# Kernel tuning notes

Hardware: AMD Instinct MI355X
Metric: run time of the kernel (lower is better)

## Reference

```python
import jax, jax.numpy as jnp
import numpy as np

D_MODEL = 2048
N_HEAD = 16
N_KV_HEAD = 4
D_HEAD = D_MODEL // N_HEAD  # 128
WINDOW = 512
B, T = 2, 2048


def _rope_tables(T, d_head, base=10000.0):
    inv = 1.0 / (base ** (np.arange(0, d_head, 2, dtype=np.float32) / d_head))
    t = np.arange(T, dtype=np.float32)
    freqs = np.outer(t, inv)  # [T, d_head//2]
    return jnp.asarray(np.cos(freqs)), jnp.asarray(np.sin(freqs))


def setup_inputs() -> dict:
    key = jax.random.key(0)
    ks = jax.random.split(key, 5)
    cos, sin = _rope_tables(T, D_HEAD)
    s = 1.0 / np.sqrt(D_MODEL)
    return {
        "x": jax.random.normal(ks[0], (B, T, D_MODEL), jnp.float32),
        "cos": cos,
        "sin": sin,
        "Wq": jax.random.normal(ks[1], (D_MODEL, D_MODEL), jnp.float32) * s,
        "Wk": jax.random.normal(ks[2], (D_MODEL, N_KV_HEAD * D_HEAD), jnp.float32) * s,
        "Wv": jax.random.normal(ks[3], (D_MODEL, N_KV_HEAD * D_HEAD), jnp.float32) * s,
        "Wo": jax.random.normal(ks[4], (D_MODEL, D_MODEL), jnp.float32) * s,
    }


def _apply_rope(t, cos, sin):
    # t: [B, T, H, D]; cos/sin: [T, D//2]; interleaved-pair (complex) rotation
    tr = t[..., 0::2]
    ti = t[..., 1::2]
    c = cos[None, :, None, :]
    s = sin[None, :, None, :]
    out_r = tr * c - ti * s
    out_i = tr * s + ti * c
    return jnp.stack([out_r, out_i], axis=-1).reshape(t.shape)


def reference(x, cos, sin, Wq, Wk, Wv, Wo):
    Bx, Tx, C = x.shape
    q = (x @ Wq).reshape(Bx, Tx, N_HEAD, D_HEAD)       # [B,T,H,D]
    k = (x @ Wk).reshape(Bx, Tx, N_KV_HEAD, D_HEAD)    # [B,T,Hkv,D]
    v = (x @ Wv).reshape(Bx, Tx, N_KV_HEAD, D_HEAD)
    q = _apply_rope(q, cos, sin)
    k = _apply_rope(k, cos, sin)
    n_rep = N_HEAD // N_KV_HEAD
    k = jnp.repeat(k, n_rep, axis=2)  # [B,T,H,D]
    v = jnp.repeat(v, n_rep, axis=2)
    scale = 1.0 / np.sqrt(D_HEAD)
    att = jnp.einsum("bihd,bjhd->bhij", q, k) * scale  # [B,H,T,T]
    i = jnp.arange(Tx)[:, None]
    j = jnp.arange(Tx)[None, :]
    mask = (j <= i) & (j >= i - WINDOW + 1)            # causal sliding window
    att = jnp.where(mask[None, None], att, -jnp.inf)
    att = jax.nn.softmax(att, axis=-1)
    y = jnp.einsum("bhij,bjhd->bihd", att, v).reshape(Bx, Tx, C)
    return y @ Wo
```

## Files before the change

kernel.cpp:

```cpp
#include <hip/hip_runtime.h>
#include <hip/hip_bf16.h>
#include <cstdint>
#include <cstddef>

#define B_ 2
#define T_ 2048
#define NH 16
#define NKV 4
#define DH 128
#define DM 2048
#define WIN 512
#define QKS 2560

typedef __attribute__((ext_vector_type(4))) float f32x4;
typedef __attribute__((ext_vector_type(8))) __bf16 bf16x8;

using bf16 = __hip_bfloat16;

__device__ inline void gload_lds16(const void* g, void* l) {
  __builtin_amdgcn_global_load_lds(
      (const __attribute__((address_space(1))) void*)g,
      (__attribute__((address_space(3))) void*)l, 16, 0, 0);
}

__device__ inline unsigned pack_bf2(float a, float b) {
  unsigned short ua = __builtin_bit_cast(unsigned short, __float2bfloat16(a));
  unsigned short ub = __builtin_bit_cast(unsigned short, __float2bfloat16(b));
  return (unsigned)ua | ((unsigned)ub << 16);
}

#define FBAR()                           \
  do {                                   \
    asm volatile("" ::: "memory");       \
    __builtin_amdgcn_s_barrier();        \
    asm volatile("" ::: "memory");       \
  } while (0)

__global__ __launch_bounds__(256) void k_prep(const float* __restrict__ x,
                                              const float* __restrict__ Wq,
                                              const float* __restrict__ Wk,
                                              const float* __restrict__ Wv,
                                              const float* __restrict__ Wo,
                                              bf16* __restrict__ xb,
                                              bf16* __restrict__ Wqkvt,
                                              bf16* __restrict__ Wot) {
  int id = blockIdx.x;
  int tid = threadIdx.x;
  if (id >= 2560) {
    size_t base = (size_t)(id - 2560) * 4096 + tid * 16;
#pragma unroll
    for (int j = 0; j < 4; ++j) {
      float4 v = *(const float4*)(x + base + j * 4);
      ushort4 o;
      o.x = __builtin_bit_cast(unsigned short, __float2bfloat16(v.x));
      o.y = __builtin_bit_cast(unsigned short, __float2bfloat16(v.y));
      o.z = __builtin_bit_cast(unsigned short, __float2bfloat16(v.z));
      o.w = __builtin_bit_cast(unsigned short, __float2bfloat16(v.w));
      *(ushort4*)(xb + base + j * 4) = o;
    }
    return;
  }
  const float* W;
  bf16* Wt;
  int N, bx, by;
  if (id < 1024) { W = Wq; Wt = Wqkvt; N = 2048; bx = id & 31; by = id >> 5; }
  else if (id < 1280) { id -= 1024; W = Wk; Wt = Wqkvt + (size_t)2048 * 2048; N = 512; bx = id & 7; by = id >> 3; }
  else if (id < 1536) { id -= 1280; W = Wv; Wt = Wqkvt + (size_t)2560 * 2048; N = 512; bx = id & 7; by = id >> 3; }
  else { id -= 1536; W = Wo; Wt = Wot; N = 2048; bx = id & 31; by = id >> 5; }

  __shared__ float tile[64][65];
  int n0 = bx * 64, k0 = by * 64;
  int tx = tid & 63, tg = tid >> 6;
#pragma unroll
  for (int r = 0; r < 16; ++r) {
    int k = tg * 16 + r;
    tile[k][tx] = W[(size_t)(k0 + k) * N + n0 + tx];
  }
  __syncthreads();
#pragma unroll
  for (int r = 0; r < 16; ++r) {
    int nn = tg * 16 + r;
    Wt[(size_t)(n0 + nn) * 2048 + k0 + tx] = __float2bfloat16(tile[tx][nn]);
  }
}

template <int BN, int EPI>
__global__ __launch_bounds__(512, 2) void k_gemm2(const bf16* __restrict__ A,
                                                  const bf16* __restrict__ Bt,
                                                  void* __restrict__ Cout,
                                                  int M, int N, int K,
                                                  const float* __restrict__ cosT,
                                                  const float* __restrict__ sinT,
                                                  bf16* __restrict__ vt) {
  constexpr int NR = BN / 64;
  __shared__ __align__(16) char As_[2][32768];
  __shared__ __align__(16) char Bs_[2][BN * 128];

  const int tid = threadIdx.x;
  const int w = tid >> 6, lane = tid & 63;
  const int li = lane & 15, g = lane >> 4;
  const int wm = w >> 2, wn = w & 3;

  const int nwg = gridDim.x * gridDim.y;
  int bid = blockIdx.y * gridDim.x + blockIdx.x;
  bid = (bid & 7) * (nwg >> 3) + (bid >> 3);
  const int m0 = (bid / gridDim.x) * 256;
  const int n0 = (bid % gridDim.x) * BN;

  const int ntiles = K >> 6;

  auto sA = [&](int buf, int tile, int half, int issue) {
    if (tile >= ntiles) return;
    const int R0 = half * 64 + issue * 128;
    const int rr = R0 + w * 8 + (lane >> 3);
    const int sl = lane & 7;
    const bf16* src = A + (size_t)(m0 + rr) * K + tile * 64 + ((sl ^ (rr & 7)) * 8);
    gload_lds16(src, As_[buf] + (R0 + w * 8) * 128);
  };
  auto sB = [&](int buf, int tile, int issue) {
    if (tile >= ntiles) return;
    const int block = issue * 8 + w;
    const int rr = block * 8 + (lane >> 3);
    const int sl = lane & 7;
    const bf16* src = Bt + (size_t)(n0 + rr) * K + tile * 64 + ((sl ^ (rr & 7)) * 8);
    gload_lds16(src, Bs_[buf] + block * 1024);
  };

  const int swz0 = (g ^ (li & 7)) * 16;
  const int swz1 = ((4 + g) ^ (li & 7)) * 16;
  bf16x8 af[8], bv[NR * 2];
  f32x4 acc[8][NR] = {};

  auto readA = [&](int buf, int mh) {
#pragma unroll
    for (int m = 0; m < 4; ++m) {
      const char* p = As_[buf] + (wm * 128 + mh * 64 + m * 16 + li) * 128;
      af[m * 2 + 0] = *(const bf16x8*)(p + swz0);
      af[m * 2 + 1] = *(const bf16x8*)(p + swz1);
    }
  };
  auto readB = [&](int buf) {
#pragma unroll
    for (int n = 0; n < NR; ++n) {
      const char* p = Bs_[buf] + (wn * (NR * 16) + n * 16 + li) * 128;
      bv[n * 2 + 0] = *(const bf16x8*)(p + swz0);
      bv[n * 2 + 1] = *(const bf16x8*)(p + swz1);
    }
  };
  auto MMA = [&](int mh) {
    __builtin_amdgcn_s_setprio(1);
#pragma unroll
    for (int m = 0; m < 4; ++m)
#pragma unroll
      for (int n = 0; n < NR; ++n)
#pragma unroll
        for (int kk = 0; kk < 2; ++kk)
          acc[mh * 4 + m][n] = __builtin_amdgcn_mfma_f32_16x16x32_bf16(
              af[m * 2 + kk], bv[n * 2 + kk], acc[mh * 4 + m][n], 0, 0, 0);
    __builtin_amdgcn_s_setprio(0);
  };
  auto VMWA = [&](bool last) {
    if (last)
      asm volatile("s_waitcnt vmcnt(0)" ::: "memory");
    else if constexpr (NR == 3)
      asm volatile("s_waitcnt vmcnt(5)" ::: "memory");
    else
      asm volatile("s_waitcnt vmcnt(4)" ::: "memory");
    __builtin_amdgcn_sched_barrier(0);
  };
  auto VMWB = [&](bool last) {
    if (last)
      asm volatile("s_waitcnt vmcnt(0)" ::: "memory");
    else
      asm volatile("s_waitcnt vmcnt(2)" ::: "memory");
    __builtin_amdgcn_sched_barrier(0);
  };

  sA(0, 0, 0, 0); sA(0, 0, 0, 1);
#pragma unroll
  for (int i = 0; i < NR; ++i) sB(0, 0, i);
  sA(0, 0, 1, 0); sA(0, 0, 1, 1);
  asm volatile("s_waitcnt vmcnt(2)" ::: "memory");
  __builtin_amdgcn_sched_barrier(0);
  FBAR();

  for (int t = 0; t < ntiles; ++t) {
    const int cb = t & 1;
    const bool last = (t == ntiles - 1);
    readA(cb, 0); readB(cb);
    sA(cb ^ 1, t + 1, 0, 0); sA(cb ^ 1, t + 1, 0, 1);
#pragma unroll
    for (int i = 0; i < NR; ++i) sB(cb ^ 1, t + 1, i);
    VMWA(last);
    FBAR(); MMA(0); FBAR();
    readA(cb, 1);
    sA(cb ^ 1, t + 1, 1, 0); sA(cb ^ 1, t + 1, 1, 1);
    VMWB(last);
    FBAR(); MMA(1); FBAR();
  }

#pragma unroll
  for (int mf = 0; mf < 8; ++mf)
#pragma unroll
    for (int nf = 0; nf < NR; ++nf) {
      const int colc = n0 + wn * (NR * 16) + nf * 16;
      const int col = colc + li;
      const int row0 = m0 + wm * 128 + mf * 16 + g * 4;
      if constexpr (EPI == 2) {
        if (colc < QKS) {
          const float qs = (colc < 2048) ? 0.08838834764831845f : 1.0f;
          const int i = (col & 127) >> 1;
          const float sgn = (li & 1) ? 1.0f : -1.0f;
#pragma unroll
          for (int r = 0; r < 4; ++r) {
            const int trow = (row0 + r) & (T_ - 1);
            float v = acc[mf][nf][r];
            float pv = __shfl_xor(v, 1);
            float c = cosT[trow * 64 + i], s = sinT[trow * 64 + i];
            float o = (v * c + pv * (sgn * s)) * qs;
            ((bf16*)Cout)[(size_t)(row0 + r) * QKS + col] = __float2bfloat16(o);
          }
        } else {
          unsigned lo = pack_bf2(acc[mf][nf][0], acc[mf][nf][1]);
          unsigned hi = pack_bf2(acc[mf][nf][2], acc[mf][nf][3]);
          uint2 pk = {lo, hi};
          *(uint2*)(vt + (size_t)(col - QKS) * (B_ * T_) + row0) = pk;
        }
      } else {
#pragma unroll
        for (int r = 0; r < 4; ++r) {
          float v = acc[mf][nf][r];
          if constexpr (EPI == 1)
            ((bf16*)Cout)[(size_t)(row0 + r) * N + col] = __float2bfloat16(v);
          else
            ((float*)Cout)[(size_t)(row0 + r) * N + col] = v;
        }
      }
    }
}

__global__ __launch_bounds__(512) void k_attn(const bf16* __restrict__ qkv,
                                              const bf16* __restrict__ vt,
                                              bf16* __restrict__ Y) {
  __shared__ __align__(16) char Ks[2][9216];
  __shared__ __align__(16) char Vs[2][10240];
  __shared__ __align__(16) char Pl[8][1280];
  const int lane = threadIdx.x & 63;
  const int w = threadIdx.x >> 6;
  const int li = lane & 15, g = lane >> 4;
  const int t0 = ((int)gridDim.x - 1 - (int)blockIdx.x) * 32;
  const int b = blockIdx.y / NKV, kvh = blockIdx.y % NKV;
  const int h = kvh * 4 + (w >> 1);
  const int qrow0 = t0 + (w & 1) * 16;
  const int t = qrow0 + li;

  bf16x8 qf[4];
  const bf16* qbase = qkv + (size_t)(b * T_ + qrow0 + li) * QKS + h * DH;
#pragma unroll
  for (int dk = 0; dk < 4; ++dk) qf[dk] = *(const bf16x8*)(qbase + dk * 32 + g * 8);

  float mrow = -1e4f;
  float srow = 0.f;
  f32x4 acc[8] = {};

  int ks0 = t0 - (WIN - 1);
  if (ks0 < 0) ks0 = 0;
  ks0 &= ~31;
  const int nt = (t0 + 31 - ks0) / 32 + 1;

  const bf16* kgbase = qkv + (size_t)(b * T_) * QKS + DM + kvh * DH;
  const bf16* vgbase = vt + (size_t)(kvh * DH) * (B_ * T_) + b * T_;

  auto STAGE = [&](int buf, int kt) {
    for (int c = w; c < 19; c += 8) {
      if (c < 9) {
        int slot = c * 64 + lane;
        int row = slot / 17, cc = slot % 17;
        if (slot >= 544) { row = 0; cc = 0; }
        if (cc == 16) cc = 0;
        const bf16* src = kgbase + (size_t)(kt + row) * QKS + cc * 8;
        gload_lds16(src, Ks[buf] + c * 1024);
      } else {
        int c2 = c - 9;
        int slot = c2 * 64 + lane;
        int row = slot / 5, cc = slot % 5;
        if (cc == 4) cc = 0;
        const bf16* src = vgbase + (size_t)row * (B_ * T_) + kt + cc * 8;
        gload_lds16(src, Vs[buf] + c2 * 1024);
      }
    }
  };

  STAGE(0, ks0);
  __syncthreads();
  int cur = 0;

  for (int it = 0; it < nt; ++it) {
    const int kt = ks0 + it * 32;
    if (it + 1 < nt) STAGE(cur ^ 1, kt + 32);

    f32x4 sc[2] = {};
#pragma unroll
    for (int n = 0; n < 2; ++n)
#pragma unroll
      for (int dk = 0; dk < 4; ++dk) {
        bf16x8 kf = *(const bf16x8*)(Ks[cur] + (n * 16 + li) * 272 + dk * 64 + g * 16);
        sc[n] = __builtin_amdgcn_mfma_f32_16x16x32_bf16(kf, qf[dk], sc[n], 0, 0, 0);
      }

    float p[2][4];
    float pmax = -1e30f;
#pragma unroll
    for (int n = 0; n < 2; ++n)
#pragma unroll
      for (int r = 0; r < 4; ++r) {
        int key = kt + n * 16 + g * 4 + r;
        bool valid = (key <= t) && (key > t - WIN);
        float pv = valid ? sc[n][r] : -1e30f;
        p[n][r] = pv;
        pmax = fmaxf(pmax, pv);
      }
    pmax = fmaxf(pmax, __shfl_xor(pmax, 16));
    pmax = fmaxf(pmax, __shfl_xor(pmax, 32));

    if (!__all(pmax <= mrow)) {
      float nm = fmaxf(mrow, pmax);
      float alpha = __expf(mrow - nm);
      mrow = nm;
      srow *= alpha;
      float af_[4];
#pragma unroll
      for (int r = 0; r < 4; ++r) af_[r] = __shfl(alpha, (g << 2) + r);
#pragma unroll
      for (int db = 0; db < 8; ++db)
#pragma unroll
        for (int r = 0; r < 4; ++r) acc[db][r] *= af_[r];
    }

    float rs = 0.f;
#pragma unroll
    for (int n = 0; n < 2; ++n)
#pragma unroll
      for (int r = 0; r < 4; ++r) {
        p[n][r] = __expf(p[n][r] - mrow);
        rs += p[n][r];
      }
    rs += __shfl_xor(rs, 16);
    rs += __shfl_xor(rs, 32);
    srow += rs;

#pragma unroll
    for (int n = 0; n < 2; ++n) {
      *(unsigned*)(Pl[w] + li * 80 + n * 32 + g * 8) = pack_bf2(p[n][0], p[n][1]);
      *(unsigned*)(Pl[w] + li * 80 + n * 32 + g * 8 + 4) = pack_bf2(p[n][2], p[n][3]);
    }

    bf16x8 pf = *(const bf16x8*)(Pl[w] + li * 80 + g * 16);
#pragma unroll
    for (int db = 0; db < 8; ++db) {
      bf16x8 vf = *(const bf16x8*)(Vs[cur] + (db * 16 + li) * 80 + g * 16);
      acc[db] = __builtin_amdgcn_mfma_f32_16x16x32_bf16(pf, vf, acc[db], 0, 0, 0);
    }

    __syncthreads();
    cur ^= 1;
  }

  float inv[4];
#pragma unroll
  for (int r = 0; r < 4; ++r) inv[r] = 1.f / __shfl(srow, (g << 2) + r);
  bf16* ybase = Y + (size_t)(b * T_ + qrow0 + (g << 2)) * DM + h * DH;
#pragma unroll
  for (int r = 0; r < 4; ++r)
#pragma unroll
    for (int db = 0; db < 8; ++db)
      ybase[(size_t)r * DM + db * 16 + li] = __float2bfloat16(acc[db][r] * inv[r]);
}

extern "C" void kernel_launch(void* const* d_in, const int* in_sizes, int n_in,
                              void* d_out, int out_size, void* d_ws, size_t ws_size,
                              hipStream_t stream) {
  const float* x = (const float*)d_in[0];
  const float* cosT = (const float*)d_in[1];
  const float* sinT = (const float*)d_in[2];
  const float* Wq = (const float*)d_in[3];
  const float* Wk = (const float*)d_in[4];
  const float* Wv = (const float*)d_in[5];
  const float* Wo = (const float*)d_in[6];
  float* out = (float*)d_out;

  char* ws = (char*)d_ws;
  bf16* xb = (bf16*)ws;     ws += (size_t)4096 * 2048 * 2;
  bf16* Wqkvt = (bf16*)ws;  ws += (size_t)3072 * 2048 * 2;
  bf16* Wot = (bf16*)ws;    ws += (size_t)2048 * 2048 * 2;
  bf16* qkv = (bf16*)ws;    ws += (size_t)4096 * QKS * 2;
  bf16* vt = (bf16*)ws;     ws += (size_t)512 * 4096 * 2;
  bf16* yb = xb;

  k_prep<<<4608, 256, 0, stream>>>(x, Wq, Wk, Wv, Wo, xb, Wqkvt, Wot);

  k_gemm2<192, 2><<<dim3(3072 / 192, 4096 / 256), 512, 0, stream>>>(
      xb, Wqkvt, qkv, 4096, 3072, 2048, cosT, sinT, vt);

  k_attn<<<dim3(T_ / 32, B_ * NKV), 512, 0, stream>>>(qkv, vt, yb);

  k_gemm2<128, 0><<<dim3(2048 / 128, 4096 / 256), 512, 0, stream>>>(
      yb, Wot, out, 4096, 2048, 2048, nullptr, nullptr, nullptr);
}
```

Before: 156.8 us.

## Reshape GEMM warp tiling and double query rows per attention wave

The GEMM changes its warp grid from 2x4 to 4x2, so each warp owns 64 rows and twice as many columns, and the A staging layout is reworked to match. The attention kernel now gives each wave two 16-row query slices sharing each K/V tile, halving the grid and reusing the staged K/V across more queries. It also skips fully masked key tiles per wave. The trade-off is more registers per thread (launch bounds of 512, 2) and fewer workgroups for the attention kernel.

```diff
diff --git a/kernel.cpp b/kernel.cpp
--- a/kernel.cpp
+++ b/kernel.cpp
@@ -92,14 +92,15 @@
                                                   const float* __restrict__ cosT,
                                                   const float* __restrict__ sinT,
                                                   bf16* __restrict__ vt) {
-  constexpr int NR = BN / 64;
+  constexpr int NR = BN / 32;
+  constexpr int NB = BN * 128 / 8192;
   __shared__ __align__(16) char As_[2][32768];
   __shared__ __align__(16) char Bs_[2][BN * 128];
 
   const int tid = threadIdx.x;
   const int w = tid >> 6, lane = tid & 63;
   const int li = lane & 15, g = lane >> 4;
-  const int wm = w >> 2, wn = w & 3;
+  const int wm = w >> 1, wn = w & 1;
 
   const int nwg = gridDim.x * gridDim.y;
   int bid = blockIdx.y * gridDim.x + blockIdx.x;
@@ -109,13 +110,13 @@
 
   const int ntiles = K >> 6;
 
-  auto sA = [&](int buf, int tile, int half, int issue) {
+  auto sA = [&](int buf, int tile, int h, int issue) {
     if (tile >= ntiles) return;
-    const int R0 = half * 64 + issue * 128;
-    const int rr = R0 + w * 8 + (lane >> 3);
-    const int sl = lane & 7;
-    const bf16* src = A + (size_t)(m0 + rr) * K + tile * 64 + ((sl ^ (rr & 7)) * 8);
-    gload_lds16(src, As_[buf] + (R0 + w * 8) * 128);
+    const int rl = issue * 64 + (tid >> 3);
+    const int row = (rl >> 5) * 64 + h * 32 + (rl & 31);
+    const int sl = tid & 7;
+    const bf16* src = A + (size_t)(m0 + row) * K + tile * 64 + ((sl ^ (rl & 7)) * 8);
+    gload_lds16(src, As_[buf] + h * 16384 + issue * 8192 + tid * 16);
   };
   auto sB = [&](int buf, int tile, int issue) {
     if (tile >= ntiles) return;
@@ -128,15 +129,16 @@
 
   const int swz0 = (g ^ (li & 7)) * 16;
   const int swz1 = ((4 + g) ^ (li & 7)) * 16;
-  bf16x8 af[8], bv[NR * 2];
-  f32x4 acc[8][NR] = {};
+  bf16x8 af[4], bv[NR * 2];
+  f32x4 acc[4][NR] = {};
 
   auto readA = [&](int buf, int mh) {
 #pragma unroll
-    for (int m = 0; m < 4; ++m) {
-      const char* p = As_[buf] + (wm * 128 + mh * 64 + m * 16 + li) * 128;
-      af[m * 2 + 0] = *(const bf16x8*)(p + swz0);
-      af[m * 2 + 1] = *(const bf16x8*)(p + swz1);
+    for (int m2 = 0; m2 < 2; ++m2) {
+      const int rl = wm * 32 + m2 * 16 + li;
+      const char* p = As_[buf] + mh * 16384 + rl * 128;
+      af[m2 * 2 + 0] = *(const bf16x8*)(p + swz0);
+      af[m2 * 2 + 1] = *(const bf16x8*)(p + swz1);
     }
   };
   auto readB = [&](int buf) {
@@ -150,62 +152,57 @@
   auto MMA = [&](int mh) {
     __builtin_amdgcn_s_setprio(1);
 #pragma unroll
-    for (int m = 0; m < 4; ++m)
+    for (int m2 = 0; m2 < 2; ++m2)
 #pragma unroll
       for (int n = 0; n < NR; ++n)
 #pragma unroll
         for (int kk = 0; kk < 2; ++kk)
-          acc[mh * 4 + m][n] = __builtin_amdgcn_mfma_f32_16x16x32_bf16(
-              af[m * 2 + kk], bv[n * 2 + kk], acc[mh * 4 + m][n], 0, 0, 0);
+          acc[mh * 2 + m2][n] = __builtin_amdgcn_mfma_f32_16x16x32_bf16(
+              af[m2 * 2 + kk], bv[n * 2 + kk], acc[mh * 2 + m2][n], 0, 0, 0);
     __builtin_amdgcn_s_setprio(0);
   };
-  auto VMWA = [&](bool last) {
-    if (last)
+
+  sA(0, 0, 0, 0); sA(0, 0, 0, 1);
+#pragma unroll
+  for (int i = 0; i < NB; ++i) sB(0, 0, i);
+  sA(0, 0, 1, 0); sA(0, 0, 1, 1);
+  asm volatile("s_waitcnt vmcnt(2)" ::: "memory");
+  __builtin_amdgcn_sched_barrier(0);
+  FBAR();
+
+  for (int t = 0; t < ntiles; ++t) {
+    const int cb = t & 1;
+    const bool last = (t == ntiles - 1);
+    readA(cb, 0); readB(cb);
+    sA(cb ^ 1, t + 1, 0, 0); sA(cb ^ 1, t + 1, 0, 1);
+#pragma unroll
+    for (int i = 0; i < NB; ++i) sB(cb ^ 1, t + 1, i);
+    if (last) {
       asm volatile("s_waitcnt vmcnt(0)" ::: "memory");
-    else if constexpr (NR == 3)
+    } else if constexpr (NB == 3) {
       asm volatile("s_waitcnt vmcnt(5)" ::: "memory");
-    else
+    } else {
       asm volatile("s_waitcnt vmcnt(4)" ::: "memory");
+    }
     __builtin_amdgcn_sched_barrier(0);
-  };
-  auto VMWB = [&](bool last) {
+    FBAR(); MMA(0); FBAR();
+    readA(cb, 1);
+    sA(cb ^ 1, t + 1, 1, 0); sA(cb ^ 1, t + 1, 1, 1);
     if (last)
       asm volatile("s_waitcnt vmcnt(0)" ::: "memory");
     else
       asm volatile("s_waitcnt vmcnt(2)" ::: "memory");
     __builtin_amdgcn_sched_barrier(0);
-  };
-
-  sA(0, 0, 0, 0); sA(0, 0, 0, 1);
-#pragma unroll
-  for (int i = 0; i < NR; ++i) sB(0, 0, i);
-  sA(0, 0, 1, 0); sA(0, 0, 1, 1);
-  asm volatile("s_waitcnt vmcnt(2)" ::: "memory");
-  __builtin_amdgcn_sched_barrier(0);
-  FBAR();
-
-  for (int t = 0; t < ntiles; ++t) {
-    const int cb = t & 1;
-    const bool last = (t == ntiles - 1);
-    readA(cb, 0); readB(cb);
-    sA(cb ^ 1, t + 1, 0, 0); sA(cb ^ 1, t + 1, 0, 1);
-#pragma unroll
-    for (int i = 0; i < NR; ++i) sB(cb ^ 1, t + 1, i);
-    VMWA(last);
-    FBAR(); MMA(0); FBAR();
-    readA(cb, 1);
-    sA(cb ^ 1, t + 1, 1, 0); sA(cb ^ 1, t + 1, 1, 1);
-    VMWB(last);
     FBAR(); MMA(1); FBAR();
   }
 
 #pragma unroll
-  for (int mf = 0; mf < 8; ++mf)
+  for (int mf = 0; mf < 4; ++mf)
 #pragma unroll
     for (int nf = 0; nf < NR; ++nf) {
       const int colc = n0 + wn * (NR * 16) + nf * 16;
       const int col = colc + li;
-      const int row0 = m0 + wm * 128 + mf * 16 + g * 4;
+      const int row0 = m0 + wm * 64 + mf * 16 + g * 4;
       if constexpr (EPI == 2) {
         if (colc < QKS) {
           const float qs = (colc < 2048) ? 0.08838834764831845f : 1.0f;
@@ -228,45 +225,42 @@
         }
       } else {
 #pragma unroll
-        for (int r = 0; r < 4; ++r) {
-          float v = acc[mf][nf][r];
-          if constexpr (EPI == 1)
-            ((bf16*)Cout)[(size_t)(row0 + r) * N + col] = __float2bfloat16(v);
-          else
-            ((float*)Cout)[(size_t)(row0 + r) * N + col] = v;
-        }
+        for (int r = 0; r < 4; ++r)
+          ((float*)Cout)[(size_t)(row0 + r) * N + col] = acc[mf][nf][r];
       }
     }
 }
 
-__global__ __launch_bounds__(512) void k_attn(const bf16* __restrict__ qkv,
-                                              const bf16* __restrict__ vt,
-                                              bf16* __restrict__ Y) {
+__global__ __launch_bounds__(512, 2) void k_attn(const bf16* __restrict__ qkv,
+                                                 const bf16* __restrict__ vt,
+                                                 bf16* __restrict__ Y) {
   __shared__ __align__(16) char Ks[2][9216];
   __shared__ __align__(16) char Vs[2][10240];
-  __shared__ __align__(16) char Pl[8][1280];
+  __shared__ __align__(16) char Pl[8][2][1280];
   const int lane = threadIdx.x & 63;
   const int w = threadIdx.x >> 6;
   const int li = lane & 15, g = lane >> 4;
-  const int t0 = ((int)gridDim.x - 1 - (int)blockIdx.x) * 32;
+  const int t0 = ((int)gridDim.x - 1 - (int)blockIdx.x) * 64;
   const int b = blockIdx.y / NKV, kvh = blockIdx.y % NKV;
   const int h = kvh * 4 + (w >> 1);
-  const int qrow0 = t0 + (w & 1) * 16;
-  const int t = qrow0 + li;
-
-  bf16x8 qf[4];
-  const bf16* qbase = qkv + (size_t)(b * T_ + qrow0 + li) * QKS + h * DH;
-#pragma unroll
-  for (int dk = 0; dk < 4; ++dk) qf[dk] = *(const bf16x8*)(qbase + dk * 32 + g * 8);
-
-  float mrow = -1e4f;
-  float srow = 0.f;
-  f32x4 acc[8] = {};
+  const int qrow0 = t0 + (w & 1) * 32;
+
+  bf16x8 qf[2][4];
+#pragma unroll
+  for (int s = 0; s < 2; ++s) {
+    const bf16* qbase = qkv + (size_t)(b * T_ + qrow0 + s * 16 + li) * QKS + h * DH;
+#pragma unroll
+    for (int dk = 0; dk < 4; ++dk) qf[s][dk] = *(const bf16x8*)(qbase + dk * 32 + g * 8);
+  }
+
+  float mrow[2] = {-1e4f, -1e4f};
+  float srow[2] = {0.f, 0.f};
+  f32x4 acc[2][8] = {};
 
   int ks0 = t0 - (WIN - 1);
   if (ks0 < 0) ks0 = 0;
   ks0 &= ~31;
-  const int nt = (t0 + 31 - ks0) / 32 + 1;
+  const int nt = (t0 + 63 - ks0) / 32 + 1;
 
   const bf16* kgbase = qkv + (size_t)(b * T_) * QKS + DM + kvh * DH;
   const bf16* vgbase = vt + (size_t)(kvh * DH) * (B_ * T_) + b * T_;
@@ -299,82 +293,94 @@
     const int kt = ks0 + it * 32;
     if (it + 1 < nt) STAGE(cur ^ 1, kt + 32);
 
-    f32x4 sc[2] = {};
-#pragma unroll
-    for (int n = 0; n < 2; ++n)
-#pragma unroll
-      for (int dk = 0; dk < 4; ++dk) {
-        bf16x8 kf = *(const bf16x8*)(Ks[cur] + (n * 16 + li) * 272 + dk * 64 + g * 16);
-        sc[n] = __builtin_amdgcn_mfma_f32_16x16x32_bf16(kf, qf[dk], sc[n], 0, 0, 0);
+    if (!(kt > qrow0 + 31 || kt + 31 < qrow0 - (WIN - 1))) {
+      f32x4 sc[2][2] = {};
+#pragma unroll
+      for (int n = 0; n < 2; ++n)
+#pragma unroll
+        for (int dk = 0; dk < 4; ++dk) {
+          bf16x8 kf = *(const bf16x8*)(Ks[cur] + (n * 16 + li) * 272 + dk * 64 + g * 16);
+          sc[0][n] = __builtin_amdgcn_mfma_f32_16x16x32_bf16(kf, qf[0][dk], sc[0][n], 0, 0, 0);
+          sc[1][n] = __builtin_amdgcn_mfma_f32_16x16x32_bf16(kf, qf[1][dk], sc[1][n], 0, 0, 0);
+        }
+
+#pragma unroll
+      for (int s = 0; s < 2; ++s) {
+        const int t = qrow0 + s * 16 + li;
+        float p[2][4];
+        float pmax = -1e30f;
+#pragma unroll
+        for (int n = 0; n < 2; ++n)
+#pragma unroll
+          for (int r = 0; r < 4; ++r) {
+            int key = kt + n * 16 + g * 4 + r;
+            bool valid = (key <= t) && (key > t - WIN);
+            float pv = valid ? sc[s][n][r] : -1e30f;
+            p[n][r] = pv;
+            pmax = fmaxf(pmax, pv);
+          }
+        pmax = fmaxf(pmax, __shfl_xor(pmax, 16));
+        pmax = fmaxf(pmax, __shfl_xor(pmax, 32));
+
+        if (!__all(pmax <= mrow[s])) {
+          float nm = fmaxf(mrow[s], pmax);
+          float alpha = __expf(mrow[s] - nm);
+          mrow[s] = nm;
+          srow[s] *= alpha;
+          float af_[4];
+#pragma unroll
+          for (int r = 0; r < 4; ++r) af_[r] = __shfl(alpha, (g << 2) + r);
+#pragma unroll
+          for (int db = 0; db < 8; ++db)
+#pragma unroll
+            for (int r = 0; r < 4; ++r) acc[s][db][r] *= af_[r];
+        }
+
+        float rs = 0.f;
+#pragma unroll
+        for (int n = 0; n < 2; ++n)
+#pragma unroll
+          for (int r = 0; r < 4; ++r) {
+            p[n][r] = __expf(p[n][r] - mrow[s]);
+            rs += p[n][r];
+          }
+        rs += __shfl_xor(rs, 16);
+        rs += __shfl_xor(rs, 32);
+        srow[s] += rs;
+
+#pragma unroll
+        for (int n = 0; n < 2; ++n) {
+          *(unsigned*)(Pl[w][s] + li * 80 + n * 32 + g * 8) = pack_bf2(p[n][0], p[n][1]);
+          *(unsigned*)(Pl[w][s] + li * 80 + n * 32 + g * 8 + 4) = pack_bf2(p[n][2], p[n][3]);
+        }
       }
 
-    float p[2][4];
-    float pmax = -1e30f;
-#pragma unroll
-    for (int n = 0; n < 2; ++n)
-#pragma unroll
-      for (int r = 0; r < 4; ++r) {
-        int key = kt + n * 16 + g * 4 + r;
-        bool valid = (key <= t) && (key > t - WIN);
-        float pv = valid ? sc[n][r] : -1e30f;
-        p[n][r] = pv;
-        pmax = fmaxf(pmax, pv);
+      bf16x8 pf0 = *(const bf16x8*)(Pl[w][0] + li * 80 + g * 16);
+      bf16x8 pf1 = *(const bf16x8*)(Pl[w][1] + li * 80 + g * 16);
+#pragma unroll
+      for (int db = 0; db < 8; ++db) {
+        bf16x8 vf = *(const bf16x8*)(Vs[cur] + (db * 16 + li) * 80 + g * 16);
+        acc[0][db] = __builtin_amdgcn_mfma_f32_16x16x32_bf16(pf0, vf, acc[0][db], 0, 0, 0);
+        acc[1][db] = __builtin_amdgcn_mfma_f32_16x16x32_bf16(pf1, vf, acc[1][db], 0, 0, 0);
       }
-    pmax = fmaxf(pmax, __shfl_xor(pmax, 16));
-    pmax = fmaxf(pmax, __shfl_xor(pmax, 32));
-
-    if (!__all(pmax <= mrow)) {
-      float nm = fmaxf(mrow, pmax);
-      float alpha = __expf(mrow - nm);
-      mrow = nm;
-      srow *= alpha;
-      float af_[4];
-#pragma unroll
-      for (int r = 0; r < 4; ++r) af_[r] = __shfl(alpha, (g << 2) + r);
-#pragma unroll
-      for (int db = 0; db < 8; ++db)
-#pragma unroll
-        for (int r = 0; r < 4; ++r) acc[db][r] *= af_[r];
-    }
-
-    float rs = 0.f;
-#pragma unroll
-    for (int n = 0; n < 2; ++n)
-#pragma unroll
-      for (int r = 0; r < 4; ++r) {
-        p[n][r] = __expf(p[n][r] - mrow);
-        rs += p[n][r];
-      }
-    rs += __shfl_xor(rs, 16);
-    rs += __shfl_xor(rs, 32);
-    srow += rs;
-
-#pragma unroll
-    for (int n = 0; n < 2; ++n) {
-      *(unsigned*)(Pl[w] + li * 80 + n * 32 + g * 8) = pack_bf2(p[n][0], p[n][1]);
-      *(unsigned*)(Pl[w] + li * 80 + n * 32 + g * 8 + 4) = pack_bf2(p[n][2], p[n][3]);
-    }
-
-    bf16x8 pf = *(const bf16x8*)(Pl[w] + li * 80 + g * 16);
-#pragma unroll
-    for (int db = 0; db < 8; ++db) {
-      bf16x8 vf = *(const bf16x8*)(Vs[cur] + (db * 16 + li) * 80 + g * 16);
-      acc[db] = __builtin_amdgcn_mfma_f32_16x16x32_bf16(pf, vf, acc[db], 0, 0, 0);
     }
 
     __syncthreads();
     cur ^= 1;
   }
 
-  float inv[4];
-#pragma unroll
-  for (int r = 0; r < 4; ++r) inv[r] = 1.f / __shfl(srow, (g << 2) + r);
-  bf16* ybase = Y + (size_t)(b * T_ + qrow0 + (g << 2)) * DM + h * DH;
-#pragma unroll
-  for (int r = 0; r < 4; ++r)
-#pragma unroll
-    for (int db = 0; db < 8; ++db)
-      ybase[(size_t)r * DM + db * 16 + li] = __float2bfloat16(acc[db][r] * inv[r]);
+#pragma unroll
+  for (int s = 0; s < 2; ++s) {
+    float inv[4];
+#pragma unroll
+    for (int r = 0; r < 4; ++r) inv[r] = 1.f / __shfl(srow[s], (g << 2) + r);
+    bf16* ybase = Y + (size_t)(b * T_ + qrow0 + s * 16 + (g << 2)) * DM + h * DH;
+#pragma unroll
+    for (int r = 0; r < 4; ++r)
+#pragma unroll
+      for (int db = 0; db < 8; ++db)
+        ybase[(size_t)r * DM + db * 16 + li] = __float2bfloat16(acc[s][db][r] * inv[r]);
+  }
 }
 
 extern "C" void kernel_launch(void* const* d_in, const int* in_sizes, int n_in,
@@ -402,7 +408,7 @@
   k_gemm2<192, 2><<<dim3(3072 / 192, 4096 / 256), 512, 0, stream>>>(
       xb, Wqkvt, qkv, 4096, 3072, 2048, cosT, sinT, vt);
 
-  k_attn<<<dim3(T_ / 32, B_ * NKV), 512, 0, stream>>>(qkv, vt, yb);
+  k_attn<<<dim3(T_ / 64, B_ * NKV), 512, 0, stream>>>(qkv, vt, yb);
 
   k_gemm2<128, 0><<<dim3(2048 / 128, 4096 / 256), 512, 0, stream>>>(
       yb, Wot, out, 4096, 2048, 2048, nullptr, nullptr, nullptr);
```

Result: slower. 161.7 us (+3.1%).

## Shrink GEMM M-tile to 128 rows and raise occupancy to four blocks

Applied to the files above, without the earlier changes.

Halves the GEMM block tile in M from 256 to 128 rows, cuts the A shared-memory buffers and per-thread accumulators in half, and rewrites the A staging layout and vmcnt waits to match. Launch bounds move from 2 to 4 blocks per CU and the grids double in the M dimension. This gives more workgroups to fill the CUs and more waves to hide latency, at the cost of less operand reuse per block and more reloading of B tiles. The unused EPI==1 bf16 store path is removed.

```diff
diff --git a/kernel.cpp b/kernel.cpp
--- a/kernel.cpp
+++ b/kernel.cpp
@@ -85,7 +85,7 @@
 }
 
 template <int BN, int EPI>
-__global__ __launch_bounds__(512, 2) void k_gemm2(const bf16* __restrict__ A,
+__global__ __launch_bounds__(512, 4) void k_gemm2(const bf16* __restrict__ A,
                                                   const bf16* __restrict__ Bt,
                                                   void* __restrict__ Cout,
                                                   int M, int N, int K,
@@ -93,7 +93,7 @@
                                                   const float* __restrict__ sinT,
                                                   bf16* __restrict__ vt) {
   constexpr int NR = BN / 64;
-  __shared__ __align__(16) char As_[2][32768];
+  __shared__ __align__(16) char As_[2][16384];
   __shared__ __align__(16) char Bs_[2][BN * 128];
 
   const int tid = threadIdx.x;
@@ -104,18 +104,18 @@
   const int nwg = gridDim.x * gridDim.y;
   int bid = blockIdx.y * gridDim.x + blockIdx.x;
   bid = (bid & 7) * (nwg >> 3) + (bid >> 3);
-  const int m0 = (bid / gridDim.x) * 256;
+  const int m0 = (bid / gridDim.x) * 128;
   const int n0 = (bid % gridDim.x) * BN;
 
   const int ntiles = K >> 6;
 
-  auto sA = [&](int buf, int tile, int half, int issue) {
+  auto sA = [&](int buf, int tile, int h) {
     if (tile >= ntiles) return;
-    const int R0 = half * 64 + issue * 128;
-    const int rr = R0 + w * 8 + (lane >> 3);
-    const int sl = lane & 7;
-    const bf16* src = A + (size_t)(m0 + rr) * K + tile * 64 + ((sl ^ (rr & 7)) * 8);
-    gload_lds16(src, As_[buf] + (R0 + w * 8) * 128);
+    const int rl = tid >> 3;
+    const int row = (rl & 31) + h * 32 + ((rl >> 5) << 6);
+    const int sl = tid & 7;
+    const bf16* src = A + (size_t)(m0 + row) * K + tile * 64 + ((sl ^ (rl & 7)) * 8);
+    gload_lds16(src, As_[buf] + h * 8192 + tid * 16);
   };
   auto sB = [&](int buf, int tile, int issue) {
     if (tile >= ntiles) return;
@@ -128,15 +128,16 @@
 
   const int swz0 = (g ^ (li & 7)) * 16;
   const int swz1 = ((4 + g) ^ (li & 7)) * 16;
-  bf16x8 af[8], bv[NR * 2];
-  f32x4 acc[8][NR] = {};
+  bf16x8 af[4], bv[NR * 2];
+  f32x4 acc[4][NR] = {};
 
   auto readA = [&](int buf, int mh) {
 #pragma unroll
-    for (int m = 0; m < 4; ++m) {
-      const char* p = As_[buf] + (wm * 128 + mh * 64 + m * 16 + li) * 128;
-      af[m * 2 + 0] = *(const bf16x8*)(p + swz0);
-      af[m * 2 + 1] = *(const bf16x8*)(p + swz1);
+    for (int m2 = 0; m2 < 2; ++m2) {
+      const int rl = wm * 32 + m2 * 16 + li;
+      const char* p = As_[buf] + mh * 8192 + rl * 128;
+      af[m2 * 2 + 0] = *(const bf16x8*)(p + swz0);
+      af[m2 * 2 + 1] = *(const bf16x8*)(p + swz1);
     }
   };
   auto readB = [&](int buf) {
@@ -150,37 +151,21 @@
   auto MMA = [&](int mh) {
     __builtin_amdgcn_s_setprio(1);
 #pragma unroll
-    for (int m = 0; m < 4; ++m)
+    for (int m2 = 0; m2 < 2; ++m2)
 #pragma unroll
       for (int n = 0; n < NR; ++n)
 #pragma unroll
         for (int kk = 0; kk < 2; ++kk)
-          acc[mh * 4 + m][n] = __builtin_amdgcn_mfma_f32_16x16x32_bf16(
-              af[m * 2 + kk], bv[n * 2 + kk], acc[mh * 4 + m][n], 0, 0, 0);
+          acc[mh * 2 + m2][n] = __builtin_amdgcn_mfma_f32_16x16x32_bf16(
+              af[m2 * 2 + kk], bv[n * 2 + kk], acc[mh * 2 + m2][n], 0, 0, 0);
     __builtin_amdgcn_s_setprio(0);
   };
-  auto VMWA = [&](bool last) {
-    if (last)
-      asm volatile("s_waitcnt vmcnt(0)" ::: "memory");
-    else if constexpr (NR == 3)
-      asm volatile("s_waitcnt vmcnt(5)" ::: "memory");
-    else
-      asm volatile("s_waitcnt vmcnt(4)" ::: "memory");
-    __builtin_amdgcn_sched_barrier(0);
-  };
-  auto VMWB = [&](bool last) {
-    if (last)
-      asm volatile("s_waitcnt vmcnt(0)" ::: "memory");
-    else
-      asm volatile("s_waitcnt vmcnt(2)" ::: "memory");
-    __builtin_amdgcn_sched_barrier(0);
-  };
-
-  sA(0, 0, 0, 0); sA(0, 0, 0, 1);
+
+  sA(0, 0, 0);
 #pragma unroll
   for (int i = 0; i < NR; ++i) sB(0, 0, i);
-  sA(0, 0, 1, 0); sA(0, 0, 1, 1);
-  asm volatile("s_waitcnt vmcnt(2)" ::: "memory");
+  sA(0, 0, 1);
+  asm volatile("s_waitcnt vmcnt(1)" ::: "memory");
   __builtin_amdgcn_sched_barrier(0);
   FBAR();
 
@@ -188,24 +173,32 @@
     const int cb = t & 1;
     const bool last = (t == ntiles - 1);
     readA(cb, 0); readB(cb);
-    sA(cb ^ 1, t + 1, 0, 0); sA(cb ^ 1, t + 1, 0, 1);
+    sA(cb ^ 1, t + 1, 0);
 #pragma unroll
     for (int i = 0; i < NR; ++i) sB(cb ^ 1, t + 1, i);
-    VMWA(last);
+    if (last)
+      asm volatile("s_waitcnt vmcnt(0)" ::: "memory");
+    else
+      asm volatile("s_waitcnt vmcnt(4)" ::: "memory");
+    __builtin_amdgcn_sched_barrier(0);
     FBAR(); MMA(0); FBAR();
     readA(cb, 1);
-    sA(cb ^ 1, t + 1, 1, 0); sA(cb ^ 1, t + 1, 1, 1);
-    VMWB(last);
+    sA(cb ^ 1, t + 1, 1);
+    if (last)
+      asm volatile("s_waitcnt vmcnt(0)" ::: "memory");
+    else
+      asm volatile("s_waitcnt vmcnt(1)" ::: "memory");
+    __builtin_amdgcn_sched_barrier(0);
     FBAR(); MMA(1); FBAR();
   }
 
 #pragma unroll
-  for (int mf = 0; mf < 8; ++mf)
+  for (int mf = 0; mf < 4; ++mf)
 #pragma unroll
     for (int nf = 0; nf < NR; ++nf) {
       const int colc = n0 + wn * (NR * 16) + nf * 16;
       const int col = colc + li;
-      const int row0 = m0 + wm * 128 + mf * 16 + g * 4;
+      const int row0 = m0 + wm * 64 + (mf >> 1) * 32 + (mf & 1) * 16 + g * 4;
       if constexpr (EPI == 2) {
         if (colc < QKS) {
           const float qs = (colc < 2048) ? 0.08838834764831845f : 1.0f;
@@ -228,13 +221,8 @@
         }
       } else {
 #pragma unroll
-        for (int r = 0; r < 4; ++r) {
-          float v = acc[mf][nf][r];
-          if constexpr (EPI == 1)
-            ((bf16*)Cout)[(size_t)(row0 + r) * N + col] = __float2bfloat16(v);
-          else
-            ((float*)Cout)[(size_t)(row0 + r) * N + col] = v;
-        }
+        for (int r = 0; r < 4; ++r)
+          ((float*)Cout)[(size_t)(row0 + r) * N + col] = acc[mf][nf][r];
       }
     }
 }
@@ -399,11 +387,11 @@
 
   k_prep<<<4608, 256, 0, stream>>>(x, Wq, Wk, Wv, Wo, xb, Wqkvt, Wot);
 
-  k_gemm2<192, 2><<<dim3(3072 / 192, 4096 / 256), 512, 0, stream>>>(
+  k_gemm2<192, 2><<<dim3(3072 / 192, 4096 / 128), 512, 0, stream>>>(
       xb, Wqkvt, qkv, 4096, 3072, 2048, cosT, sinT, vt);
 
   k_attn<<<dim3(T_ / 32, B_ * NKV), 512, 0, stream>>>(qkv, vt, yb);
 
-  k_gemm2<128, 0><<<dim3(2048 / 128, 4096 / 256), 512, 0, stream>>>(
+  k_gemm2<128, 0><<<dim3(2048 / 128, 4096 / 128), 512, 0, stream>>>(
       yb, Wot, out, 4096, 2048, 2048, nullptr, nullptr, nullptr);
 }
```

New measurement: 159.4 us. Within noise of the previous version (+1.6%).
